# Performance work log

Measured on AMD Instinct MI355X. Metric: run time of the kernel, lower is better.

Reference implementation:

```python
import jax, jax.numpy as jnp
import numpy as np

N = 50000        # nodes
E = 800000       # edges
D_IN = 64        # input_dim
D_E = 16         # edge_dim
D_OUT = 64       # output_dim
HEADS = 8
HEAD_DIM = D_OUT // HEADS
COMB = 2 * D_IN + D_E  # 144


def _linear_init(key, fan_in, fan_out):
    kw, kb = jax.random.split(key)
    lim = 1.0 / np.sqrt(fan_in)
    W = jax.random.uniform(kw, (fan_in, fan_out), minval=-lim, maxval=lim, dtype=jnp.float32)
    b = jax.random.uniform(kb, (fan_out,), minval=-lim, maxval=lim, dtype=jnp.float32)
    return W, b


def setup_inputs() -> dict:
    key = jax.random.key(0)
    ks = jax.random.split(key, 16)
    inp = {
        "x": jax.random.normal(ks[0], (N, D_IN), dtype=jnp.float32),
        "edge_attr": jax.random.normal(ks[1], (E, D_E), dtype=jnp.float32),
        "edge_index": jax.random.randint(ks[2], (2, E), 0, N, dtype=jnp.int32),
        "q": jax.random.uniform(ks[3], (1, D_OUT), dtype=jnp.float32) * 0.1,
    }
    # three ResidualStacks: k (COMB->D_OUT), v (COMB->D_OUT), out (D_OUT->D_OUT)
    for pre, fan_in, kbase in (("k", COMB, 4), ("v", COMB, 8), ("o", D_OUT, 12)):
        W0, b0 = _linear_init(ks[kbase], fan_in, D_OUT)
        W1, b1 = _linear_init(ks[kbase + 1], D_OUT, D_OUT)
        W2, b2 = _linear_init(ks[kbase + 2], D_OUT, D_OUT)
        inp.update({f"{pre}_W0": W0, f"{pre}_b0": b0,
                    f"{pre}_W1": W1, f"{pre}_b1": b1,
                    f"{pre}_W2": W2, f"{pre}_b2": b2})
    return inp


def residual_stack(h, W0, b0, W1, b1, W2, b2, last_activation):
    # input projection + ReLU, then 2 residual linear blocks
    h = jax.nn.relu(h @ W0 + b0)
    h = jax.nn.relu(h + h @ W1 + b1)
    h = h + h @ W2 + b2
    if last_activation:
        h = jax.nn.relu(h)
    return h


def neighborhood_attention(q, k, v, index):
    # q: (1, D_OUT), k/v: (E, D_OUT), index: (E,) destination node ids
    kh = k.reshape(E, HEADS, HEAD_DIM)
    qh = q.reshape(1, HEADS, HEAD_DIM)
    scores = jnp.sum(qh * kh, axis=-1) / np.sqrt(HEAD_DIM)  # (E, HEADS)
    m = jax.ops.segment_max(scores, index, num_segments=N)  # (N, HEADS)
    ex = jnp.exp(scores - jax.lax.stop_gradient(m)[index])
    denom = jax.ops.segment_sum(ex, index, num_segments=N)  # (N, HEADS)
    alpha = ex / denom[index]
    vh = v.reshape(E, HEADS, HEAD_DIM)
    return (alpha[:, :, None] * vh).reshape(E, D_OUT)


def reference(x, edge_attr, edge_index, q,
              k_W0, k_b0, k_W1, k_b1, k_W2, k_b2,
              v_W0, v_b0, v_W1, v_b1, v_W2, v_b2,
              o_W0, o_b0, o_W1, o_b1, o_W2, o_b2):
    src, dst = edge_index[0], edge_index[1]
    feat = jnp.concatenate([x[src], x[dst], edge_attr], axis=-1)  # (E, COMB)
    k = residual_stack(feat, k_W0, k_b0, k_W1, k_b1, k_W2, k_b2, last_activation=False)
    v = residual_stack(feat, v_W0, v_b0, v_W1, v_b1, v_W2, v_b2, last_activation=False)
    messages = neighborhood_attention(q, k, v, dst)               # (E, D_OUT)
    aggr = jax.ops.segment_sum(messages, dst, num_segments=N)    # (N, D_OUT)
    out = residual_stack(jax.nn.relu(aggr), o_W0, o_b0, o_W1, o_b1, o_W2, o_b2, last_activation=False)
    # skip_connection=True, input_dim == output_dim -> identity skip
    return jax.nn.relu(x + out)
```

## Files before the change

### kernel.cpp

```cpp
#include <hip/hip_runtime.h>

#define N_NODES 50000
#define E_EDGES 800000
#define D_OUT   64
#define COMB    144

typedef float  f32x4  __attribute__((ext_vector_type(4)));
typedef __bf16 bf16x8 __attribute__((ext_vector_type(8)));
typedef __bf16 bf16x4 __attribute__((ext_vector_type(4)));

#define WS_NUM_OFF   0
#define WS_DEN_OFF   (12800000)
#define WS_WTS_OFF   (14400000)
#define BIG_ELEMS    (64*168)
#define SMALL_ELEMS  (64*72)

__global__ __launch_bounds__(256) void prep_kernel(
    const float* __restrict__ kW0, const float* __restrict__ kW1, const float* __restrict__ kW2,
    const float* __restrict__ vW0, const float* __restrict__ vW1, const float* __restrict__ vW2,
    const float* __restrict__ oW0, const float* __restrict__ oW1, const float* __restrict__ oW2,
    __bf16* __restrict__ wout)
{
    const int b = blockIdx.x, tid = threadIdx.x;
    const float* src;
    __bf16* dst;
    int K, Kpad, lb;
    if (b < 42)      { src = kW0; dst = wout;             K = 144; Kpad = 168; lb = b; }
    else if (b < 84) { src = vW0; dst = wout + BIG_ELEMS; K = 144; Kpad = 168; lb = b - 42; }
    else {
        const int id = (b - 84) / 18; lb = (b - 84) % 18;
        const float* s7[7] = {kW1, kW2, vW1, vW2, oW0, oW1, oW2};
        src = s7[id]; dst = wout + 2 * BIG_ELEMS + id * SMALL_ELEMS;
        K = 64; Kpad = 72;
    }
    const int idx = lb * 256 + tid;
    const int col = idx / Kpad, k = idx % Kpad;
    dst[idx] = (k < K) ? (__bf16)src[k * 64 + col] : (__bf16)0.f;
}

__device__ __forceinline__ void gemm64(const __bf16* Arow, const __bf16* Wt,
                                       int hi, int row16, f32x4 acc[4])
{
    #pragma unroll
    for (int kc = 0; kc < 2; ++kc) {
        const bf16x8 a = *(const bf16x8*)(Arow + kc * 32 + hi * 8);
        #pragma unroll
        for (int n = 0; n < 4; ++n) {
            const bf16x8 bfr = *(const bf16x8*)(Wt + (n * 16 + row16) * 72 + kc * 32 + hi * 8);
            acc[n] = __builtin_amdgcn_mfma_f32_16x16x32_bf16(a, bfr, acc[n], 0, 0, 0);
        }
    }
}

__device__ __forceinline__ bf16x8 pack8(float4 a, float4 b) {
    bf16x8 r;
    r[0] = (__bf16)a.x; r[1] = (__bf16)a.y; r[2] = (__bf16)a.z; r[3] = (__bf16)a.w;
    r[4] = (__bf16)b.x; r[5] = (__bf16)b.y; r[6] = (__bf16)b.z; r[7] = (__bf16)b.w;
    return r;
}

__global__ __launch_bounds__(256, 6) void edge_kernel(
    const float* __restrict__ x,
    const float* __restrict__ edge_attr,
    const int*   __restrict__ edge_index,
    const float* __restrict__ q,
    const float* __restrict__ kb0, const float* __restrict__ kb1, const float* __restrict__ kb2,
    const float* __restrict__ vb0, const float* __restrict__ vb1, const float* __restrict__ vb2,
    const __bf16* __restrict__ kW0t, const __bf16* __restrict__ kW1t, const __bf16* __restrict__ kW2t,
    const __bf16* __restrict__ vW0t, const __bf16* __restrict__ vW1t, const __bf16* __restrict__ vW2t,
    float* __restrict__ num, float* __restrict__ den)
{
    __shared__ __bf16 H_s[64][72];

    const int tid   = threadIdx.x;
    const int lane  = tid & 63;
    const int w     = tid >> 6;
    const int row16 = lane & 15;
    const int hi    = lane >> 4;
    const int wrow  = w * 16;

    const int e0 = (blockIdx.x * 4 + w) * 16;
    const int er = e0 + row16;

    const int src  = edge_index[er];
    const int dstn = edge_index[E_EDGES + er];

    bf16x8 af[5];
    {
        const float* xs = &x[(size_t)src * 64 + hi * 8];
        af[0] = pack8(*(const float4*)xs,        *(const float4*)(xs + 4));
        af[1] = pack8(*(const float4*)(xs + 32), *(const float4*)(xs + 36));
        const float* xd = &x[(size_t)dstn * 64 + hi * 8];
        af[2] = pack8(*(const float4*)xd,        *(const float4*)(xd + 4));
        af[3] = pack8(*(const float4*)(xd + 32), *(const float4*)(xd + 36));
        if (hi < 2) {
            const float* ep = &edge_attr[(size_t)er * 16 + hi * 8];
            af[4] = pack8(*(const float4*)ep, *(const float4*)(ep + 4));
        } else {
            #pragma unroll
            for (int i = 0; i < 8; ++i) af[4][i] = (__bf16)0.f;
        }
    }

    const __bf16* hrow = &H_s[wrow + row16][0];
    float ex[4][4];

    {
        f32x4 acc[4] = {{0,0,0,0},{0,0,0,0},{0,0,0,0},{0,0,0,0}};
        #pragma unroll
        for (int kc = 0; kc < 5; ++kc) {
            #pragma unroll
            for (int n = 0; n < 4; ++n) {
                const bf16x8 bfr = *(const bf16x8*)(kW0t + (n * 16 + row16) * 168 + kc * 32 + hi * 8);
                acc[n] = __builtin_amdgcn_mfma_f32_16x16x32_bf16(af[kc], bfr, acc[n], 0, 0, 0);
            }
        }
        float h0[4][4];
        #pragma unroll
        for (int n = 0; n < 4; ++n) {
            const float bias = kb0[n * 16 + row16];
            #pragma unroll
            for (int r = 0; r < 4; ++r) {
                h0[n][r] = fmaxf(acc[n][r] + bias, 0.f);
                H_s[wrow + hi * 4 + r][n * 16 + row16] = (__bf16)h0[n][r];
            }
        }
        __builtin_amdgcn_wave_barrier();

        f32x4 acc1[4] = {{0,0,0,0},{0,0,0,0},{0,0,0,0},{0,0,0,0}};
        gemm64(hrow, kW1t, hi, row16, acc1);
        float h1[4][4];
        #pragma unroll
        for (int n = 0; n < 4; ++n) {
            const float bias = kb1[n * 16 + row16];
            #pragma unroll
            for (int r = 0; r < 4; ++r) {
                h1[n][r] = fmaxf(h0[n][r] + acc1[n][r] + bias, 0.f);
                H_s[wrow + hi * 4 + r][n * 16 + row16] = (__bf16)h1[n][r];
            }
        }
        __builtin_amdgcn_wave_barrier();

        f32x4 acc2[4] = {{0,0,0,0},{0,0,0,0},{0,0,0,0},{0,0,0,0}};
        gemm64(hrow, kW2t, hi, row16, acc2);

        #pragma unroll
        for (int n = 0; n < 4; ++n) {
            const float bias = kb2[n * 16 + row16];
            const float qv   = q[n * 16 + row16];
            #pragma unroll
            for (int r = 0; r < 4; ++r) {
                const float kk = h1[n][r] + acc2[n][r] + bias;
                float p = qv * kk;
                p += __shfl_xor(p, 1);
                p += __shfl_xor(p, 2);
                p += __shfl_xor(p, 4);
                ex[n][r] = __expf(p * 0.35355339059327373f);
            }
        }
    }

    float vv[4][4];
    {
        f32x4 acc[4] = {{0,0,0,0},{0,0,0,0},{0,0,0,0},{0,0,0,0}};
        #pragma unroll
        for (int kc = 0; kc < 5; ++kc) {
            #pragma unroll
            for (int n = 0; n < 4; ++n) {
                const bf16x8 bfr = *(const bf16x8*)(vW0t + (n * 16 + row16) * 168 + kc * 32 + hi * 8);
                acc[n] = __builtin_amdgcn_mfma_f32_16x16x32_bf16(af[kc], bfr, acc[n], 0, 0, 0);
            }
        }
        float h0[4][4];
        #pragma unroll
        for (int n = 0; n < 4; ++n) {
            const float bias = vb0[n * 16 + row16];
            #pragma unroll
            for (int r = 0; r < 4; ++r) {
                h0[n][r] = fmaxf(acc[n][r] + bias, 0.f);
                H_s[wrow + hi * 4 + r][n * 16 + row16] = (__bf16)h0[n][r];
            }
        }
        __builtin_amdgcn_wave_barrier();

        f32x4 acc1[4] = {{0,0,0,0},{0,0,0,0},{0,0,0,0},{0,0,0,0}};
        gemm64(hrow, vW1t, hi, row16, acc1);
        float h1[4][4];
        #pragma unroll
        for (int n = 0; n < 4; ++n) {
            const float bias = vb1[n * 16 + row16];
            #pragma unroll
            for (int r = 0; r < 4; ++r) {
                h1[n][r] = fmaxf(h0[n][r] + acc1[n][r] + bias, 0.f);
                H_s[wrow + hi * 4 + r][n * 16 + row16] = (__bf16)h1[n][r];
            }
        }
        __builtin_amdgcn_wave_barrier();

        f32x4 acc2[4] = {{0,0,0,0},{0,0,0,0},{0,0,0,0},{0,0,0,0}};
        gemm64(hrow, vW2t, hi, row16, acc2);
        #pragma unroll
        for (int n = 0; n < 4; ++n) {
            const float bias = vb2[n * 16 + row16];
            #pragma unroll
            for (int r = 0; r < 4; ++r)
                vv[n][r] = h1[n][r] + acc2[n][r] + bias;
        }
    }

    const int b3 = row16 >> 3;
    #pragma unroll
    for (int r = 0; r < 4; ++r) {
        const int drow = __shfl(dstn, hi * 4 + r);
        if ((lane & 7) == 0) {
            #pragma unroll
            for (int n = 0; n < 4; ++n)
                atomicAdd(&den[(size_t)drow * 8 + 2 * n + b3], ex[n][r]);
        }
        #pragma unroll
        for (int n = 0; n < 4; ++n)
            atomicAdd(&num[(size_t)drow * 64 + n * 16 + row16], ex[n][r] * vv[n][r]);
    }
}

__global__ __launch_bounds__(256) void node_kernel(
    const float* __restrict__ x,
    const float* __restrict__ num, const float* __restrict__ den,
    const float* __restrict__ ob0, const float* __restrict__ ob1, const float* __restrict__ ob2,
    const __bf16* __restrict__ oW0t, const __bf16* __restrict__ oW1t, const __bf16* __restrict__ oW2t,
    float* __restrict__ out)
{
    __shared__ __bf16 A_s[64][72];
    __shared__ __bf16 H_s[64][72];

    const int tid  = threadIdx.x;
    const int lane = tid & 63;
    const int w    = tid >> 6;
    const int n0   = blockIdx.x * 64;
    const int row16 = lane & 15;
    const int hi    = lane >> 4;

    for (int i = tid; i < 64 * 16; i += 256) {
        const int r = i >> 4, cc = (i & 15) * 4;
        const int node = n0 + r;
        bf16x4 h; h[0] = h[1] = h[2] = h[3] = (__bf16)0.f;
        if (node < N_NODES) {
            const float dh = den[(size_t)node * 8 + (cc >> 3)];
            if (dh > 0.f) {
                const float4 f = *(const float4*)&num[(size_t)node * 64 + cc];
                const float inv = 1.f / dh;
                h[0] = (__bf16)fmaxf(f.x * inv, 0.f);
                h[1] = (__bf16)fmaxf(f.y * inv, 0.f);
                h[2] = (__bf16)fmaxf(f.z * inv, 0.f);
                h[3] = (__bf16)fmaxf(f.w * inv, 0.f);
            }
        }
        *(bf16x4*)&A_s[r][cc] = h;
    }
    __syncthreads();

    const __bf16* arow = &A_s[w * 16 + row16][0];
    const __bf16* hrow = &H_s[w * 16 + row16][0];

    f32x4 acc[4] = {{0,0,0,0},{0,0,0,0},{0,0,0,0},{0,0,0,0}};
    gemm64(arow, oW0t, hi, row16, acc);
    float h0[4][4];
    #pragma unroll
    for (int n = 0; n < 4; ++n) {
        const float bias = ob0[n * 16 + row16];
        #pragma unroll
        for (int r = 0; r < 4; ++r) {
            h0[n][r] = fmaxf(acc[n][r] + bias, 0.f);
            H_s[w * 16 + hi * 4 + r][n * 16 + row16] = (__bf16)h0[n][r];
        }
    }
    __builtin_amdgcn_wave_barrier();

    f32x4 acc1[4] = {{0,0,0,0},{0,0,0,0},{0,0,0,0},{0,0,0,0}};
    gemm64(hrow, oW1t, hi, row16, acc1);
    float h1[4][4];
    #pragma unroll
    for (int n = 0; n < 4; ++n) {
        const float bias = ob1[n * 16 + row16];
        #pragma unroll
        for (int r = 0; r < 4; ++r) {
            h1[n][r] = fmaxf(h0[n][r] + acc1[n][r] + bias, 0.f);
            H_s[w * 16 + hi * 4 + r][n * 16 + row16] = (__bf16)h1[n][r];
        }
    }
    __builtin_amdgcn_wave_barrier();

    f32x4 acc2[4] = {{0,0,0,0},{0,0,0,0},{0,0,0,0},{0,0,0,0}};
    gemm64(hrow, oW2t, hi, row16, acc2);
    #pragma unroll
    for (int n = 0; n < 4; ++n) {
        const float bias = ob2[n * 16 + row16];
        #pragma unroll
        for (int r = 0; r < 4; ++r) {
            const int node = n0 + w * 16 + hi * 4 + r;
            if (node < N_NODES) {
                const int col = n * 16 + row16;
                const float o = h1[n][r] + acc2[n][r] + bias;
                out[(size_t)node * 64 + col] = fmaxf(x[(size_t)node * 64 + col] + o, 0.f);
            }
        }
    }
}

extern "C" void kernel_launch(void* const* d_in, const int* in_sizes, int n_in,
                              void* d_out, int out_size, void* d_ws, size_t ws_size,
                              hipStream_t stream) {
    const float* x  = (const float*)d_in[0];
    const float* ea = (const float*)d_in[1];
    const int*   ei = (const int*)d_in[2];
    const float* q  = (const float*)d_in[3];
    const float* kW0 = (const float*)d_in[4];  const float* kb0 = (const float*)d_in[5];
    const float* kW1 = (const float*)d_in[6];  const float* kb1 = (const float*)d_in[7];
    const float* kW2 = (const float*)d_in[8];  const float* kb2 = (const float*)d_in[9];
    const float* vW0 = (const float*)d_in[10]; const float* vb0 = (const float*)d_in[11];
    const float* vW1 = (const float*)d_in[12]; const float* vb1 = (const float*)d_in[13];
    const float* vW2 = (const float*)d_in[14]; const float* vb2 = (const float*)d_in[15];
    const float* oW0 = (const float*)d_in[16]; const float* ob0 = (const float*)d_in[17];
    const float* oW1 = (const float*)d_in[18]; const float* ob1 = (const float*)d_in[19];
    const float* oW2 = (const float*)d_in[20]; const float* ob2 = (const float*)d_in[21];

    char* ws = (char*)d_ws;
    float*  num  = (float*)(ws + WS_NUM_OFF);
    float*  den  = (float*)(ws + WS_DEN_OFF);
    __bf16* wts  = (__bf16*)(ws + WS_WTS_OFF);
    __bf16* kW0t = wts;
    __bf16* vW0t = wts + BIG_ELEMS;
    __bf16* sm   = wts + 2 * BIG_ELEMS;
    __bf16* kW1t = sm;                   __bf16* kW2t = sm + SMALL_ELEMS;
    __bf16* vW1t = sm + 2 * SMALL_ELEMS; __bf16* vW2t = sm + 3 * SMALL_ELEMS;
    __bf16* oW0t = sm + 4 * SMALL_ELEMS; __bf16* oW1t = sm + 5 * SMALL_ELEMS;
    __bf16* oW2t = sm + 6 * SMALL_ELEMS;

    hipMemsetAsync(d_ws, 0, (size_t)N_NODES * (64 + 8) * sizeof(float), stream);

    prep_kernel<<<210, 256, 0, stream>>>(kW0, kW1, kW2, vW0, vW1, vW2, oW0, oW1, oW2, wts);

    edge_kernel<<<E_EDGES / 64, 256, 0, stream>>>(
        x, ea, ei, q,
        kb0, kb1, kb2, vb0, vb1, vb2,
        kW0t, kW1t, kW2t, vW0t, vW1t, vW2t,
        num, den);

    node_kernel<<<(N_NODES + 63) / 64, 256, 0, stream>>>(
        x, num, den, ob0, ob1, ob2, oW0t, oW1t, oW2t, (float*)d_out);
}
```

Measured before the change: 453.2 us.

## Replace atomic scatter aggregation with CSR bucketing and per-node gather reduction

Builds a destination CSR on the device each call: a degree count, a single-block scan and a cursor. The edge kernel then writes each edge's bf16 message and exp weights into a slot grouped by destination instead of issuing fp32 atomics on num/den. A new gather kernel sums each node's messages, normalises and applies ReLU, and the node MLP reads the bf16 aggregate. This path runs only when the workspace is large enough, otherwise the old atomic path is used. It trades many float atomics for an extra large message buffer write and read, a serial single-block scan, bf16 rounding of messages, and higher launch-bounds occupancy.

```diff
diff --git a/kernel.cpp b/kernel.cpp
--- a/kernel.cpp
+++ b/kernel.cpp
@@ -9,9 +9,17 @@
 typedef __bf16 bf16x8 __attribute__((ext_vector_type(8)));
 typedef __bf16 bf16x4 __attribute__((ext_vector_type(4)));
 
+#define CSR_DEG_OFF    0
+#define CSR_START_OFF  200192
+#define CSR_CURSOR_OFF 400384
+#define CSR_WTS_OFF    600576
+#define CSR_AGGR_OFF   708096
+#define CSR_MSG_OFF    7108096
+#define CSR_WS_NEED    122308096ULL
 #define WS_NUM_OFF   0
 #define WS_DEN_OFF   (12800000)
 #define WS_WTS_OFF   (14400000)
+
 #define BIG_ELEMS    (64*168)
 #define SMALL_ELEMS  (64*72)
 
@@ -38,6 +46,54 @@
     dst[idx] = (k < K) ? (__bf16)src[k * 64 + col] : (__bf16)0.f;
 }
 
+__global__ __launch_bounds__(256) void deg_kernel(const int* __restrict__ edge_index,
+                                                  int* __restrict__ deg)
+{
+    const int e = blockIdx.x * 256 + threadIdx.x;
+    if (e < E_EDGES) atomicAdd(&deg[edge_index[E_EDGES + e]], 1);
+}
+
+__global__ __launch_bounds__(1024) void scan_kernel(const int* __restrict__ deg,
+                                                    int* __restrict__ start,
+                                                    int* __restrict__ cursor)
+{
+    __shared__ int wsum[16];
+    __shared__ int carry_s;
+    const int tid = threadIdx.x, lane = tid & 63, wv = tid >> 6;
+    if (tid == 0) carry_s = 0;
+    __syncthreads();
+    for (int base = 0; base < N_NODES; base += 1024) {
+        const int i = base + tid;
+        const int v = (i < N_NODES) ? deg[i] : 0;
+        int sc = v;
+        #pragma unroll
+        for (int off = 1; off < 64; off <<= 1) {
+            int t = __shfl_up(sc, off);
+            if (lane >= off) sc += t;
+        }
+        if (lane == 63) wsum[wv] = sc;
+        const int c = carry_s;
+        __syncthreads();
+        if (wv == 0 && lane < 16) {
+            int ws = wsum[lane];
+            #pragma unroll
+            for (int off = 1; off < 16; off <<= 1) {
+                int t = __shfl_up(ws, off);
+                if (lane >= off) ws += t;
+            }
+            wsum[lane] = ws;
+        }
+        __syncthreads();
+        const int woff = (wv == 0) ? 0 : wsum[wv - 1];
+        const int excl = c + woff + sc - v;
+        if (i < N_NODES) { start[i] = excl; cursor[i] = excl; }
+        __syncthreads();
+        if (tid == 0) carry_s = c + wsum[15];
+        __syncthreads();
+    }
+    if (tid == 0) start[N_NODES] = carry_s;
+}
+
 __device__ __forceinline__ void gemm64(const __bf16* Arow, const __bf16* Wt,
                                        int hi, int row16, f32x4 acc[4])
 {
@@ -59,7 +115,7 @@
     return r;
 }
 
-__global__ __launch_bounds__(256, 6) void edge_kernel(
+__global__ __launch_bounds__(256, 8) void edge_kernel_csr(
     const float* __restrict__ x,
     const float* __restrict__ edge_attr,
     const int*   __restrict__ edge_index,
@@ -68,7 +124,7 @@
     const float* __restrict__ vb0, const float* __restrict__ vb1, const float* __restrict__ vb2,
     const __bf16* __restrict__ kW0t, const __bf16* __restrict__ kW1t, const __bf16* __restrict__ kW2t,
     const __bf16* __restrict__ vW0t, const __bf16* __restrict__ vW1t, const __bf16* __restrict__ vW2t,
-    float* __restrict__ num, float* __restrict__ den)
+    int* __restrict__ cursor, __bf16* __restrict__ msg)
 {
     __shared__ __bf16 H_s[64][72];
 
@@ -84,6 +140,9 @@
 
     const int src  = edge_index[er];
     const int dstn = edge_index[E_EDGES + er];
+
+    int slot = 0;
+    if (hi == 0) slot = atomicAdd(&cursor[dstn], 1);
 
     bf16x8 af[5];
     {
@@ -208,6 +267,269 @@
         }
     }
 
+    #pragma unroll
+    for (int r = 0; r < 4; ++r) {
+        const int erow = hi * 4 + r;
+        const int sl   = __shfl(slot, erow);
+        __bf16* mrow = msg + (size_t)sl * 72;
+        #pragma unroll
+        for (int n = 0; n < 4; ++n)
+            mrow[n * 16 + row16] = (__bf16)(ex[n][r] * vv[n][r]);
+        if ((row16 & 7) == 0) {
+            #pragma unroll
+            for (int n = 0; n < 4; ++n)
+                mrow[64 + 2 * n + (row16 >> 3)] = (__bf16)ex[n][r];
+        }
+    }
+}
+
+__global__ __launch_bounds__(256, 8) void aggr_kernel(
+    const int* __restrict__ start, const __bf16* __restrict__ msg,
+    __bf16* __restrict__ aggrb)
+{
+    const int lane = threadIdx.x & 63;
+    const int n    = blockIdx.x * 4 + (threadIdx.x >> 6);
+    if (n >= N_NODES) return;
+    int s = start[n];
+    const int e = start[n + 1];
+    float accm = 0.f, acce = 0.f;
+    for (; s + 1 < e; s += 2) {
+        const size_t b0 = (size_t)s * 72, b1 = b0 + 72;
+        const float m0 = (float)msg[b0 + lane];
+        const float e0 = (float)msg[b0 + 64 + (lane >> 3)];
+        const float m1 = (float)msg[b1 + lane];
+        const float e1 = (float)msg[b1 + 64 + (lane >> 3)];
+        accm += m0 + m1; acce += e0 + e1;
+    }
+    if (s < e) {
+        const size_t b0 = (size_t)s * 72;
+        accm += (float)msg[b0 + lane];
+        acce += (float)msg[b0 + 64 + (lane >> 3)];
+    }
+    const float a = (acce > 0.f) ? fmaxf(accm / acce, 0.f) : 0.f;
+    aggrb[(size_t)n * 64 + lane] = (__bf16)a;
+}
+
+__global__ __launch_bounds__(256) void node_kernel_csr(
+    const float* __restrict__ x, const __bf16* __restrict__ aggrb,
+    const float* __restrict__ ob0, const float* __restrict__ ob1, const float* __restrict__ ob2,
+    const __bf16* __restrict__ oW0t, const __bf16* __restrict__ oW1t, const __bf16* __restrict__ oW2t,
+    float* __restrict__ out)
+{
+    __shared__ __bf16 A_s[64][72];
+    __shared__ __bf16 H_s[64][72];
+
+    const int tid  = threadIdx.x;
+    const int lane = tid & 63;
+    const int w    = tid >> 6;
+    const int n0   = blockIdx.x * 64;
+    const int row16 = lane & 15;
+    const int hi    = lane >> 4;
+
+    {
+        const int r = tid >> 2, seg = tid & 3;
+        const int node = n0 + r;
+        bf16x8 v0, v1;
+        #pragma unroll
+        for (int i = 0; i < 8; ++i) { v0[i] = (__bf16)0.f; v1[i] = (__bf16)0.f; }
+        if (node < N_NODES) {
+            v0 = *(const bf16x8*)&aggrb[(size_t)node * 64 + seg * 16];
+            v1 = *(const bf16x8*)&aggrb[(size_t)node * 64 + seg * 16 + 8];
+        }
+        *(bf16x8*)&A_s[r][seg * 16]     = v0;
+        *(bf16x8*)&A_s[r][seg * 16 + 8] = v1;
+    }
+    __syncthreads();
+
+    const __bf16* arow = &A_s[w * 16 + row16][0];
+    const __bf16* hrow = &H_s[w * 16 + row16][0];
+
+    f32x4 acc[4] = {{0,0,0,0},{0,0,0,0},{0,0,0,0},{0,0,0,0}};
+    gemm64(arow, oW0t, hi, row16, acc);
+    float h0[4][4];
+    #pragma unroll
+    for (int n = 0; n < 4; ++n) {
+        const float bias = ob0[n * 16 + row16];
+        #pragma unroll
+        for (int r = 0; r < 4; ++r) {
+            h0[n][r] = fmaxf(acc[n][r] + bias, 0.f);
+            H_s[w * 16 + hi * 4 + r][n * 16 + row16] = (__bf16)h0[n][r];
+        }
+    }
+    __builtin_amdgcn_wave_barrier();
+
+    f32x4 acc1[4] = {{0,0,0,0},{0,0,0,0},{0,0,0,0},{0,0,0,0}};
+    gemm64(hrow, oW1t, hi, row16, acc1);
+    float h1[4][4];
+    #pragma unroll
+    for (int n = 0; n < 4; ++n) {
+        const float bias = ob1[n * 16 + row16];
+        #pragma unroll
+        for (int r = 0; r < 4; ++r) {
+            h1[n][r] = fmaxf(h0[n][r] + acc1[n][r] + bias, 0.f);
+            H_s[w * 16 + hi * 4 + r][n * 16 + row16] = (__bf16)h1[n][r];
+        }
+    }
+    __builtin_amdgcn_wave_barrier();
+
+    f32x4 acc2[4] = {{0,0,0,0},{0,0,0,0},{0,0,0,0},{0,0,0,0}};
+    gemm64(hrow, oW2t, hi, row16, acc2);
+    #pragma unroll
+    for (int n = 0; n < 4; ++n) {
+        const float bias = ob2[n * 16 + row16];
+        #pragma unroll
+        for (int r = 0; r < 4; ++r) {
+            const int node = n0 + w * 16 + hi * 4 + r;
+            if (node < N_NODES) {
+                const int col = n * 16 + row16;
+                const float o = h1[n][r] + acc2[n][r] + bias;
+                out[(size_t)node * 64 + col] = fmaxf(x[(size_t)node * 64 + col] + o, 0.f);
+            }
+        }
+    }
+}
+
+__global__ __launch_bounds__(256, 6) void edge_kernel_atomic(
+    const float* __restrict__ x,
+    const float* __restrict__ edge_attr,
+    const int*   __restrict__ edge_index,
+    const float* __restrict__ q,
+    const float* __restrict__ kb0, const float* __restrict__ kb1, const float* __restrict__ kb2,
+    const float* __restrict__ vb0, const float* __restrict__ vb1, const float* __restrict__ vb2,
+    const __bf16* __restrict__ kW0t, const __bf16* __restrict__ kW1t, const __bf16* __restrict__ kW2t,
+    const __bf16* __restrict__ vW0t, const __bf16* __restrict__ vW1t, const __bf16* __restrict__ vW2t,
+    float* __restrict__ num, float* __restrict__ den)
+{
+    __shared__ __bf16 H_s[64][72];
+
+    const int tid   = threadIdx.x;
+    const int lane  = tid & 63;
+    const int w     = tid >> 6;
+    const int row16 = lane & 15;
+    const int hi    = lane >> 4;
+    const int wrow  = w * 16;
+
+    const int e0 = (blockIdx.x * 4 + w) * 16;
+    const int er = e0 + row16;
+
+    const int src  = edge_index[er];
+    const int dstn = edge_index[E_EDGES + er];
+
+    bf16x8 af[5];
+    {
+        const float* xs = &x[(size_t)src * 64 + hi * 8];
+        af[0] = pack8(*(const float4*)xs,        *(const float4*)(xs + 4));
+        af[1] = pack8(*(const float4*)(xs + 32), *(const float4*)(xs + 36));
+        const float* xd = &x[(size_t)dstn * 64 + hi * 8];
+        af[2] = pack8(*(const float4*)xd,        *(const float4*)(xd + 4));
+        af[3] = pack8(*(const float4*)(xd + 32), *(const float4*)(xd + 36));
+        if (hi < 2) {
+            const float* ep = &edge_attr[(size_t)er * 16 + hi * 8];
+            af[4] = pack8(*(const float4*)ep, *(const float4*)(ep + 4));
+        } else {
+            #pragma unroll
+            for (int i = 0; i < 8; ++i) af[4][i] = (__bf16)0.f;
+        }
+    }
+
+    const __bf16* hrow = &H_s[wrow + row16][0];
+    float ex[4][4];
+    {
+        f32x4 acc[4] = {{0,0,0,0},{0,0,0,0},{0,0,0,0},{0,0,0,0}};
+        #pragma unroll
+        for (int kc = 0; kc < 5; ++kc) {
+            #pragma unroll
+            for (int n = 0; n < 4; ++n) {
+                const bf16x8 bfr = *(const bf16x8*)(kW0t + (n * 16 + row16) * 168 + kc * 32 + hi * 8);
+                acc[n] = __builtin_amdgcn_mfma_f32_16x16x32_bf16(af[kc], bfr, acc[n], 0, 0, 0);
+            }
+        }
+        float h0[4][4];
+        #pragma unroll
+        for (int n = 0; n < 4; ++n) {
+            const float bias = kb0[n * 16 + row16];
+            #pragma unroll
+            for (int r = 0; r < 4; ++r) {
+                h0[n][r] = fmaxf(acc[n][r] + bias, 0.f);
+                H_s[wrow + hi * 4 + r][n * 16 + row16] = (__bf16)h0[n][r];
+            }
+        }
+        __builtin_amdgcn_wave_barrier();
+        f32x4 acc1[4] = {{0,0,0,0},{0,0,0,0},{0,0,0,0},{0,0,0,0}};
+        gemm64(hrow, kW1t, hi, row16, acc1);
+        float h1[4][4];
+        #pragma unroll
+        for (int n = 0; n < 4; ++n) {
+            const float bias = kb1[n * 16 + row16];
+            #pragma unroll
+            for (int r = 0; r < 4; ++r) {
+                h1[n][r] = fmaxf(h0[n][r] + acc1[n][r] + bias, 0.f);
+                H_s[wrow + hi * 4 + r][n * 16 + row16] = (__bf16)h1[n][r];
+            }
+        }
+        __builtin_amdgcn_wave_barrier();
+        f32x4 acc2[4] = {{0,0,0,0},{0,0,0,0},{0,0,0,0},{0,0,0,0}};
+        gemm64(hrow, kW2t, hi, row16, acc2);
+        #pragma unroll
+        for (int n = 0; n < 4; ++n) {
+            const float bias = kb2[n * 16 + row16];
+            const float qv   = q[n * 16 + row16];
+            #pragma unroll
+            for (int r = 0; r < 4; ++r) {
+                const float kk = h1[n][r] + acc2[n][r] + bias;
+                float p = qv * kk;
+                p += __shfl_xor(p, 1);
+                p += __shfl_xor(p, 2);
+                p += __shfl_xor(p, 4);
+                ex[n][r] = __expf(p * 0.35355339059327373f);
+            }
+        }
+    }
+    float vv[4][4];
+    {
+        f32x4 acc[4] = {{0,0,0,0},{0,0,0,0},{0,0,0,0},{0,0,0,0}};
+        #pragma unroll
+        for (int kc = 0; kc < 5; ++kc) {
+            #pragma unroll
+            for (int n = 0; n < 4; ++n) {
+                const bf16x8 bfr = *(const bf16x8*)(vW0t + (n * 16 + row16) * 168 + kc * 32 + hi * 8);
+                acc[n] = __builtin_amdgcn_mfma_f32_16x16x32_bf16(af[kc], bfr, acc[n], 0, 0, 0);
+            }
+        }
+        float h0[4][4];
+        #pragma unroll
+        for (int n = 0; n < 4; ++n) {
+            const float bias = vb0[n * 16 + row16];
+            #pragma unroll
+            for (int r = 0; r < 4; ++r) {
+                h0[n][r] = fmaxf(acc[n][r] + bias, 0.f);
+                H_s[wrow + hi * 4 + r][n * 16 + row16] = (__bf16)h0[n][r];
+            }
+        }
+        __builtin_amdgcn_wave_barrier();
+        f32x4 acc1[4] = {{0,0,0,0},{0,0,0,0},{0,0,0,0},{0,0,0,0}};
+        gemm64(hrow, vW1t, hi, row16, acc1);
+        float h1[4][4];
+        #pragma unroll
+        for (int n = 0; n < 4; ++n) {
+            const float bias = vb1[n * 16 + row16];
+            #pragma unroll
+            for (int r = 0; r < 4; ++r) {
+                h1[n][r] = fmaxf(h0[n][r] + acc1[n][r] + bias, 0.f);
+                H_s[wrow + hi * 4 + r][n * 16 + row16] = (__bf16)h1[n][r];
+            }
+        }
+        __builtin_amdgcn_wave_barrier();
+        f32x4 acc2[4] = {{0,0,0,0},{0,0,0,0},{0,0,0,0},{0,0,0,0}};
+        gemm64(hrow, vW2t, hi, row16, acc2);
+        #pragma unroll
+        for (int n = 0; n < 4; ++n) {
+            const float bias = vb2[n * 16 + row16];
+            #pragma unroll
+            for (int r = 0; r < 4; ++r)
+                vv[n][r] = h1[n][r] + acc2[n][r] + bias;
+        }
+    }
     const int b3 = row16 >> 3;
     #pragma unroll
     for (int r = 0; r < 4; ++r) {
@@ -223,7 +545,7 @@
     }
 }
 
-__global__ __launch_bounds__(256) void node_kernel(
+__global__ __launch_bounds__(256) void node_kernel_atomic(
     const float* __restrict__ x,
     const float* __restrict__ num, const float* __restrict__ den,
     const float* __restrict__ ob0, const float* __restrict__ ob1, const float* __restrict__ ob2,
@@ -325,27 +647,58 @@
     const float* oW2 = (const float*)d_in[20]; const float* ob2 = (const float*)d_in[21];
 
     char* ws = (char*)d_ws;
-    float*  num  = (float*)(ws + WS_NUM_OFF);
-    float*  den  = (float*)(ws + WS_DEN_OFF);
-    __bf16* wts  = (__bf16*)(ws + WS_WTS_OFF);
-    __bf16* kW0t = wts;
-    __bf16* vW0t = wts + BIG_ELEMS;
-    __bf16* sm   = wts + 2 * BIG_ELEMS;
-    __bf16* kW1t = sm;                   __bf16* kW2t = sm + SMALL_ELEMS;
-    __bf16* vW1t = sm + 2 * SMALL_ELEMS; __bf16* vW2t = sm + 3 * SMALL_ELEMS;
-    __bf16* oW0t = sm + 4 * SMALL_ELEMS; __bf16* oW1t = sm + 5 * SMALL_ELEMS;
-    __bf16* oW2t = sm + 6 * SMALL_ELEMS;
-
-    hipMemsetAsync(d_ws, 0, (size_t)N_NODES * (64 + 8) * sizeof(float), stream);
-
-    prep_kernel<<<210, 256, 0, stream>>>(kW0, kW1, kW2, vW0, vW1, vW2, oW0, oW1, oW2, wts);
-
-    edge_kernel<<<E_EDGES / 64, 256, 0, stream>>>(
-        x, ea, ei, q,
-        kb0, kb1, kb2, vb0, vb1, vb2,
-        kW0t, kW1t, kW2t, vW0t, vW1t, vW2t,
-        num, den);
-
-    node_kernel<<<(N_NODES + 63) / 64, 256, 0, stream>>>(
-        x, num, den, ob0, ob1, ob2, oW0t, oW1t, oW2t, (float*)d_out);
-}
+
+    if (ws_size >= CSR_WS_NEED) {
+        int*    deg    = (int*)(ws + CSR_DEG_OFF);
+        int*    start  = (int*)(ws + CSR_START_OFF);
+        int*    cursor = (int*)(ws + CSR_CURSOR_OFF);
+        __bf16* wts    = (__bf16*)(ws + CSR_WTS_OFF);
+        __bf16* aggrb  = (__bf16*)(ws + CSR_AGGR_OFF);
+        __bf16* msg    = (__bf16*)(ws + CSR_MSG_OFF);
+
+        __bf16* kW0t = wts;
+        __bf16* vW0t = wts + BIG_ELEMS;
+        __bf16* sm   = wts + 2 * BIG_ELEMS;
+        __bf16* kW1t = sm;                   __bf16* kW2t = sm + SMALL_ELEMS;
+        __bf16* vW1t = sm + 2 * SMALL_ELEMS; __bf16* vW2t = sm + 3 * SMALL_ELEMS;
+        __bf16* oW0t = sm + 4 * SMALL_ELEMS; __bf16* oW1t = sm + 5 * SMALL_ELEMS;
+        __bf16* oW2t = sm + 6 * SMALL_ELEMS;
+
+        hipMemsetAsync(deg, 0, (size_t)N_NODES * sizeof(int), stream);
+        deg_kernel<<<E_EDGES / 256, 256, 0, stream>>>(ei, deg);
+        scan_kernel<<<1, 1024, 0, stream>>>(deg, start, cursor);
+        prep_kernel<<<210, 256, 0, stream>>>(kW0, kW1, kW2, vW0, vW1, vW2, oW0, oW1, oW2, wts);
+
+        edge_kernel_csr<<<E_EDGES / 64, 256, 0, stream>>>(
+            x, ea, ei, q,
+            kb0, kb1, kb2, vb0, vb1, vb2,
+            kW0t, kW1t, kW2t, vW0t, vW1t, vW2t,
+            cursor, msg);
+
+        aggr_kernel<<<(N_NODES + 3) / 4, 256, 0, stream>>>(start, msg, aggrb);
+
+        node_kernel_csr<<<(N_NODES + 63) / 64, 256, 0, stream>>>(
+            x, aggrb, ob0, ob1, ob2, oW0t, oW1t, oW2t, (float*)d_out);
+    } else {
+        float*  num  = (float*)(ws + WS_NUM_OFF);
+        float*  den  = (float*)(ws + WS_DEN_OFF);
+        __bf16* wts  = (__bf16*)(ws + WS_WTS_OFF);
+        __bf16* kW0t = wts;
+        __bf16* vW0t = wts + BIG_ELEMS;
+        __bf16* sm   = wts + 2 * BIG_ELEMS;
+        __bf16* kW1t = sm;                   __bf16* kW2t = sm + SMALL_ELEMS;
+        __bf16* vW1t = sm + 2 * SMALL_ELEMS; __bf16* vW2t = sm + 3 * SMALL_ELEMS;
+        __bf16* oW0t = sm + 4 * SMALL_ELEMS; __bf16* oW1t = sm + 5 * SMALL_ELEMS;
+        __bf16* oW2t = sm + 6 * SMALL_ELEMS;
+
+        hipMemsetAsync(ws, 0, (size_t)N_NODES * (64 + 8) * sizeof(float), stream);
+        prep_kernel<<<210, 256, 0, stream>>>(kW0, kW1, kW2, vW0, vW1, vW2, oW0, oW1, oW2, wts);
+        edge_kernel_atomic<<<E_EDGES / 64, 256, 0, stream>>>(
+            x, ea, ei, q,
+            kb0, kb1, kb2, vb0, vb1, vb2,
+            kW0t, kW1t, kW2t, vW0t, vW1t, vW2t,
+            num, den);
+        node_kernel_atomic<<<(N_NODES + 63) / 64, 256, 0, stream>>>(
+            x, num, den, ob0, ob1, ob2, oW0t, oW1t, oW2t, (float*)d_out);
+    }
+}
```

Result: slower. 589.0 us (+30.0%).

## Sort edges by destination via counting sort and remap blocks per XCD

Applied to the files above, without the earlier changes.

Adds degree-count, prefix-scan and permutation kernels that build a destination-sorted edge order. The edge kernel then processes edges in that order, with block indices remapped so that each XCD handles a contiguous range of tiles. The goal is better locality for the x[dst] gathers and for the atomic scatter into num/den, with less atomic contention spread across L2 slices. In exchange it adds three kernels (one of them a single-block serial scan), an extra indirection through perm, and atomics on the same node that now sit close together in time.

```diff
diff --git a/kernel.cpp b/kernel.cpp
--- a/kernel.cpp
+++ b/kernel.cpp
@@ -4,14 +4,19 @@
 #define E_EDGES 800000
 #define D_OUT   64
 #define COMB    144
+#define NTILES  (E_EDGES / 64)
 
 typedef float  f32x4  __attribute__((ext_vector_type(4)));
 typedef __bf16 bf16x8 __attribute__((ext_vector_type(8)));
 typedef __bf16 bf16x4 __attribute__((ext_vector_type(4)));
 
-#define WS_NUM_OFF   0
-#define WS_DEN_OFF   (12800000)
-#define WS_WTS_OFF   (14400000)
+#define WS_DEG     0
+#define WS_CURSOR  200704
+#define WS_PERM    401408
+#define WS_WTS     3601408
+#define WS_NUM     3708928
+#define WS_DEN     16508928
+
 #define BIG_ELEMS    (64*168)
 #define SMALL_ELEMS  (64*72)
 
@@ -38,6 +43,62 @@
     dst[idx] = (k < K) ? (__bf16)src[k * 64 + col] : (__bf16)0.f;
 }
 
+__global__ __launch_bounds__(256) void deg_kernel(const int* __restrict__ edge_index,
+                                                  int* __restrict__ deg)
+{
+    const int e = blockIdx.x * 256 + threadIdx.x;
+    if (e < E_EDGES) atomicAdd(&deg[edge_index[E_EDGES + e]], 1);
+}
+
+__global__ __launch_bounds__(1024) void scan_kernel(const int* __restrict__ deg,
+                                                    int* __restrict__ cursor)
+{
+    __shared__ int wsum[16];
+    __shared__ int carry_s;
+    const int tid = threadIdx.x, lane = tid & 63, wv = tid >> 6;
+    if (tid == 0) carry_s = 0;
+    __syncthreads();
+    for (int base = 0; base < N_NODES; base += 1024) {
+        const int i = base + tid;
+        const int v = (i < N_NODES) ? deg[i] : 0;
+        int sc = v;
+        #pragma unroll
+        for (int off = 1; off < 64; off <<= 1) {
+            int t = __shfl_up(sc, off);
+            if (lane >= off) sc += t;
+        }
+        if (lane == 63) wsum[wv] = sc;
+        const int c = carry_s;
+        __syncthreads();
+        if (wv == 0 && lane < 16) {
+            int ws = wsum[lane];
+            #pragma unroll
+            for (int off = 1; off < 16; off <<= 1) {
+                int t = __shfl_up(ws, off);
+                if (lane >= off) ws += t;
+            }
+            wsum[lane] = ws;
+        }
+        __syncthreads();
+        const int woff = (wv == 0) ? 0 : wsum[wv - 1];
+        if (i < N_NODES) cursor[i] = c + woff + sc - v;
+        __syncthreads();
+        if (tid == 0) carry_s = c + wsum[15];
+        __syncthreads();
+    }
+}
+
+__global__ __launch_bounds__(256) void perm_kernel(const int* __restrict__ edge_index,
+                                                   int* __restrict__ cursor,
+                                                   int* __restrict__ perm)
+{
+    const int e = blockIdx.x * 256 + threadIdx.x;
+    if (e < E_EDGES) {
+        const int d = edge_index[E_EDGES + e];
+        perm[atomicAdd(&cursor[d], 1)] = e;
+    }
+}
+
 __device__ __forceinline__ void gemm64(const __bf16* Arow, const __bf16* Wt,
                                        int hi, int row16, f32x4 acc[4])
 {
@@ -63,6 +124,7 @@
     const float* __restrict__ x,
     const float* __restrict__ edge_attr,
     const int*   __restrict__ edge_index,
+    const int*   __restrict__ perm,
     const float* __restrict__ q,
     const float* __restrict__ kb0, const float* __restrict__ kb1, const float* __restrict__ kb2,
     const float* __restrict__ vb0, const float* __restrict__ vb1, const float* __restrict__ vb2,
@@ -79,8 +141,14 @@
     const int hi    = lane >> 4;
     const int wrow  = w * 16;
 
-    const int e0 = (blockIdx.x * 4 + w) * 16;
-    const int er = e0 + row16;
+    const int xcd = blockIdx.x & 7, bi = blockIdx.x >> 3;
+    const int st  = (xcd < (NTILES & 7)
+                       ? xcd * ((NTILES >> 3) + 1)
+                       : (NTILES & 7) * ((NTILES >> 3) + 1) + (xcd - (NTILES & 7)) * (NTILES >> 3))
+                    + bi;
+
+    const int p  = (st * 4 + w) * 16 + row16;
+    const int er = perm[p];
 
     const int src  = edge_index[er];
     const int dstn = edge_index[E_EDGES + er];
@@ -151,11 +219,11 @@
             #pragma unroll
             for (int r = 0; r < 4; ++r) {
                 const float kk = h1[n][r] + acc2[n][r] + bias;
-                float p = qv * kk;
-                p += __shfl_xor(p, 1);
-                p += __shfl_xor(p, 2);
-                p += __shfl_xor(p, 4);
-                ex[n][r] = __expf(p * 0.35355339059327373f);
+                float p2 = qv * kk;
+                p2 += __shfl_xor(p2, 1);
+                p2 += __shfl_xor(p2, 2);
+                p2 += __shfl_xor(p2, 4);
+                ex[n][r] = __expf(p2 * 0.35355339059327373f);
             }
         }
     }
@@ -325,9 +393,13 @@
     const float* oW2 = (const float*)d_in[20]; const float* ob2 = (const float*)d_in[21];
 
     char* ws = (char*)d_ws;
-    float*  num  = (float*)(ws + WS_NUM_OFF);
-    float*  den  = (float*)(ws + WS_DEN_OFF);
-    __bf16* wts  = (__bf16*)(ws + WS_WTS_OFF);
+    int*    deg    = (int*)(ws + WS_DEG);
+    int*    cursor = (int*)(ws + WS_CURSOR);
+    int*    perm   = (int*)(ws + WS_PERM);
+    __bf16* wts    = (__bf16*)(ws + WS_WTS);
+    float*  num    = (float*)(ws + WS_NUM);
+    float*  den    = (float*)(ws + WS_DEN);
+
     __bf16* kW0t = wts;
     __bf16* vW0t = wts + BIG_ELEMS;
     __bf16* sm   = wts + 2 * BIG_ELEMS;
@@ -336,12 +408,17 @@
     __bf16* oW0t = sm + 4 * SMALL_ELEMS; __bf16* oW1t = sm + 5 * SMALL_ELEMS;
     __bf16* oW2t = sm + 6 * SMALL_ELEMS;
 
-    hipMemsetAsync(d_ws, 0, (size_t)N_NODES * (64 + 8) * sizeof(float), stream);
+    hipMemsetAsync(deg, 0, (size_t)N_NODES * sizeof(int), stream);
+    hipMemsetAsync(num, 0, (size_t)N_NODES * (64 + 8) * sizeof(float), stream);
+
+    deg_kernel<<<E_EDGES / 256, 256, 0, stream>>>(ei, deg);
+    scan_kernel<<<1, 1024, 0, stream>>>(deg, cursor);
+    perm_kernel<<<E_EDGES / 256, 256, 0, stream>>>(ei, cursor, perm);
 
     prep_kernel<<<210, 256, 0, stream>>>(kW0, kW1, kW2, vW0, vW1, vW2, oW0, oW1, oW2, wts);
 
-    edge_kernel<<<E_EDGES / 64, 256, 0, stream>>>(
-        x, ea, ei, q,
+    edge_kernel<<<NTILES, 256, 0, stream>>>(
+        x, ea, ei, perm, q,
         kb0, kb1, kb2, vb0, vb1, vb2,
         kW0t, kW1t, kW2t, vW0t, vW1t, vW2t,
         num, den);
```

Result: slower. 1.221 ms (+169.4%).
